# Optimization experiments

Measured on AMD Instinct MI355X. Metric: run time of the kernel, lower is better.

## Reference

```python
import jax, jax.numpy as jnp
import numpy as np

ALPHA = 0.25
GAMMA = 2.0


def calc_iou(a, b):
    # a: [A,4] anchors, b: [M,4] gt boxes -> IoU [A,M]
    area_b = (b[:, 2] - b[:, 0]) * (b[:, 3] - b[:, 1])
    iw = jnp.clip(jnp.minimum(a[:, None, 2], b[None, :, 2]) - jnp.maximum(a[:, None, 0], b[None, :, 0]), 0.0)
    ih = jnp.clip(jnp.minimum(a[:, None, 3], b[None, :, 3]) - jnp.maximum(a[:, None, 1], b[None, :, 1]), 0.0)
    inter = iw * ih
    area_a = (a[:, 2] - a[:, 0]) * (a[:, 3] - a[:, 1])
    ua = jnp.clip(area_a[:, None] + area_b[None, :] - inter, 1e-8)
    return inter / ua


def _per_image(classification, regression, annotation, anchor):
    valid = annotation[:, 4] != -1.0                      # padded GT mask
    has_valid = valid.any()
    cls = jnp.clip(classification, 1e-4, 1.0 - 1e-4)

    iou = calc_iou(anchor, annotation[:, :4])             # [A,M]
    iou = jnp.where(valid[None, :], iou, -1.0)            # mask padded GTs
    iou_max = iou.max(axis=1)
    iou_arg = iou.argmax(axis=1)
    assigned = annotation[iou_arg]                        # [A,5]

    pos = iou_max >= 0.5
    num_pos = pos.sum().astype(cls.dtype)

    K = classification.shape[1]
    t = jnp.full_like(classification, -1.0)
    t = jnp.where((iou_max < 0.4)[:, None], 0.0, t)
    onehot = jax.nn.one_hot(assigned[:, 4].astype(jnp.int32), K, dtype=cls.dtype)
    t = jnp.where(pos[:, None], onehot, t)

    alpha_factor = jnp.where(t == 1.0, ALPHA, 1.0 - ALPHA)
    focal_w = alpha_factor * jnp.where(t == 1.0, 1.0 - cls, cls) ** GAMMA
    bce = -(t * jnp.log(cls) + (1.0 - t) * jnp.log(1.0 - cls))
    cls_loss = jnp.where(t != -1.0, focal_w * bce, 0.0)
    cls_total = cls_loss.sum() / jnp.maximum(num_pos, 1.0)
    cls_total = jnp.where(has_valid, cls_total, 0.0)

    aw = anchor[:, 2] - anchor[:, 0]
    ah = anchor[:, 3] - anchor[:, 1]
    acx = anchor[:, 0] + 0.5 * aw
    acy = anchor[:, 1] + 0.5 * ah
    gw_raw = assigned[:, 2] - assigned[:, 0]
    gh_raw = assigned[:, 3] - assigned[:, 1]
    gcx = assigned[:, 0] + 0.5 * gw_raw                   # ctr uses unclamped w/h (as in torch)
    gcy = assigned[:, 1] + 0.5 * gh_raw
    gw = jnp.maximum(gw_raw, 1.0)
    gh = jnp.maximum(gh_raw, 1.0)
    tdx = (gcx - acx) / aw
    tdy = (gcy - acy) / ah
    tdw = jnp.log(gw / aw)
    tdh = jnp.log(gh / ah)
    norm = jnp.array([0.1, 0.1, 0.2, 0.2], dtype=cls.dtype)
    treg = jnp.stack([tdx, tdy, tdw, tdh], axis=1) / norm  # [A,4]

    diff = jnp.abs(treg - regression)
    sl1 = jnp.where(diff <= 1.0 / 9.0, 0.5 * 9.0 * diff ** 2, diff - 0.5 / 9.0)
    reg_sum = (sl1 * pos[:, None].astype(cls.dtype)).sum()
    reg_total = jnp.where(num_pos > 0.0, reg_sum / jnp.maximum(num_pos * 4.0, 1.0), 0.0)
    return cls_total, reg_total


def setup_inputs() -> dict:
    key = jax.random.key(0)
    k1, k2, k3, k4, k5, k6, k7 = jax.random.split(key, 7)
    B, A, K, M = 8, 120000, 80, 32
    classifications = jax.random.uniform(k1, (B, A, K), dtype=jnp.float32, minval=0.001, maxval=0.999)
    regressions = jax.random.normal(k2, (B, A, 4), dtype=jnp.float32)
    # anchors: valid x1y1x2y2 boxes in an ~800px image
    a_xy = jax.random.uniform(k3, (A, 2), dtype=jnp.float32, minval=0.0, maxval=600.0)
    a_wh = jax.random.uniform(k4, (A, 2), dtype=jnp.float32, minval=16.0, maxval=256.0)
    anchors = jnp.concatenate([a_xy, a_xy + a_wh], axis=1)[None]  # [1,A,4]
    # annotations: all valid GT boxes with class labels in [0,K)
    g_xy = jax.random.uniform(k5, (B, M, 2), dtype=jnp.float32, minval=0.0, maxval=500.0)
    g_wh = jax.random.uniform(k6, (B, M, 2), dtype=jnp.float32, minval=10.0, maxval=220.0)
    labels = jax.random.randint(k7, (B, M, 1), 0, K).astype(jnp.float32)
    annotations = jnp.concatenate([g_xy, g_xy + g_wh, labels], axis=2)  # [B,M,5]
    return {"classifications": classifications, "regressions": regressions,
            "anchors": anchors, "annotations": annotations}


def reference(classifications, regressions, anchors, annotations):
    anchor = anchors[0]
    cls_l, reg_l = jax.vmap(_per_image, in_axes=(0, 0, 0, None))(
        classifications, regressions, annotations, anchor)
    return cls_l.mean(keepdims=True), reg_l.mean(keepdims=True)
```

## Files before the change

### kernel.cpp

```cpp
#include <hip/hip_runtime.h>


__global__ __launch_bounds__(256) void stageA_kernel(
    const float* __restrict__ anchors,
    const float* __restrict__ regressions,
    const float* __restrict__ annotations,
    int* __restrict__ meta,
    float* __restrict__ reg_sum,
    unsigned int* __restrict__ npos,
    int A, int M)
{
    const int b = blockIdx.y;
    const int a = blockIdx.x * blockDim.x + threadIdx.x;

    __shared__ float ann[512];
    const int nl = M * 5;
    for (int i = threadIdx.x; i < nl; i += blockDim.x)
        ann[i] = annotations[b * nl + i];
    __syncthreads();

    float regl = 0.0f;
    float posf = 0.0f;

    if (a < A) {
        const float4 ab = *reinterpret_cast<const float4*>(anchors + (size_t)a * 4);
        const float aw = ab.z - ab.x, ah = ab.w - ab.y;
        const float areaA = aw * ah;

        float best = -3.0e38f;
        int arg = 0;
        for (int m = 0; m < M; ++m) {
            const float bx1 = ann[m * 5 + 0], by1 = ann[m * 5 + 1];
            const float bx2 = ann[m * 5 + 2], by2 = ann[m * 5 + 3];
            const float lb  = ann[m * 5 + 4];
            float iw = fmaxf(fminf(ab.z, bx2) - fmaxf(ab.x, bx1), 0.0f);
            float ih = fmaxf(fminf(ab.w, by2) - fmaxf(ab.y, by1), 0.0f);
            float inter = iw * ih;
            float ua = fmaxf(areaA + (bx2 - bx1) * (by2 - by1) - inter, 1e-8f);
            float iou = inter / ua;
            iou = (lb != -1.0f) ? iou : -1.0f;
            if (iou > best) { best = iou; arg = m; }
        }

        int mv;
        if (best >= 0.5f) {
            mv = (int)ann[arg * 5 + 4];
            posf = 1.0f;
            const float4 rg = *reinterpret_cast<const float4*>(
                regressions + ((size_t)b * A + a) * 4);
            const float gx1 = ann[arg * 5 + 0], gy1 = ann[arg * 5 + 1];
            const float gx2 = ann[arg * 5 + 2], gy2 = ann[arg * 5 + 3];
            const float acx = ab.x + 0.5f * aw, acy = ab.y + 0.5f * ah;
            const float gwr = gx2 - gx1, ghr = gy2 - gy1;
            const float gcx = gx1 + 0.5f * gwr, gcy = gy1 + 0.5f * ghr;
            const float gw = fmaxf(gwr, 1.0f), gh = fmaxf(ghr, 1.0f);
            const float t0 = ((gcx - acx) / aw) / 0.1f;
            const float t1 = ((gcy - acy) / ah) / 0.1f;
            const float t2 = logf(gw / aw) / 0.2f;
            const float t3 = logf(gh / ah) / 0.2f;
            const float d0 = fabsf(t0 - rg.x), d1 = fabsf(t1 - rg.y);
            const float d2 = fabsf(t2 - rg.z), d3 = fabsf(t3 - rg.w);
            const float th = 1.0f / 9.0f, c = 0.5f / 9.0f;
            regl  = (d0 <= th) ? 4.5f * d0 * d0 : d0 - c;
            regl += (d1 <= th) ? 4.5f * d1 * d1 : d1 - c;
            regl += (d2 <= th) ? 4.5f * d2 * d2 : d2 - c;
            regl += (d3 <= th) ? 4.5f * d3 * d3 : d3 - c;
        } else if (best < 0.4f) {
            mv = -1;
        } else {
            mv = -2;
        }
        meta[(size_t)b * A + a] = mv;
    }

    #pragma unroll
    for (int off = 32; off > 0; off >>= 1) {
        regl += __shfl_down(regl, off, 64);
        posf += __shfl_down(posf, off, 64);
    }
    __shared__ float wred[8];
    const int wave = threadIdx.x >> 6;
    const int lane = threadIdx.x & 63;
    if (lane == 0) { wred[wave] = regl; wred[4 + wave] = posf; }
    __syncthreads();
    if (threadIdx.x == 0) {
        const float r = wred[0] + wred[1] + wred[2] + wred[3];
        const float p = wred[4] + wred[5] + wred[6] + wred[7];
        if (r != 0.0f) atomicAdd(&reg_sum[b], r);
        if (p != 0.0f) atomicAdd(&npos[b], (unsigned int)p);
    }
}

template <int KV>
__global__ __launch_bounds__(256) void stageB_kernel(
    const float* __restrict__ cls,
    const int* __restrict__ meta,
    float* __restrict__ cls_sum,
    int A)
{
    const int b = blockIdx.y;
    const size_t nvec = (size_t)A * KV;
    const float4* __restrict__ base =
        reinterpret_cast<const float4*>(cls + (size_t)b * A * (KV * 4));
    const int* __restrict__ mbase = meta + (size_t)b * A;

    float acc = 0.0f;
    const unsigned int stride = gridDim.x * blockDim.x;
    for (size_t v = (size_t)blockIdx.x * blockDim.x + threadIdx.x; v < nvec; v += stride) {
        const float4 c4 = base[v];
        const unsigned int vu = (unsigned int)v;
        const int a = (int)(vu / KV);
        const int kbase = (int)(vu % KV) * 4;
        const int mv = mbase[a];
        if (mv != -2) {
            const float cv[4] = {c4.x, c4.y, c4.z, c4.w};
            #pragma unroll
            for (int j = 0; j < 4; ++j) {
                const float cc = fminf(fmaxf(cv[j], 1e-4f), 0.9999f);
                const bool t1 = (mv == kbase + j);
                const float x = t1 ? cc : (1.0f - cc);
                const float w = t1 ? 0.25f * (1.0f - cc) * (1.0f - cc)
                                   : 0.75f * cc * cc;
                acc += w * (-__logf(x));
            }
        }
    }

    #pragma unroll
    for (int off = 32; off > 0; off >>= 1)
        acc += __shfl_down(acc, off, 64);
    __shared__ float wred[4];
    const int wave = threadIdx.x >> 6;
    const int lane = threadIdx.x & 63;
    if (lane == 0) wred[wave] = acc;
    __syncthreads();
    if (threadIdx.x == 0)
        atomicAdd(&cls_sum[b], wred[0] + wred[1] + wred[2] + wred[3]);
}

__global__ __launch_bounds__(256) void stageB_generic(
    const float* __restrict__ cls, const int* __restrict__ meta,
    float* __restrict__ cls_sum, int A, int K)
{
    const int b = blockIdx.y;
    const int kv = K / 4;
    const size_t nvec = (size_t)A * kv;
    const float4* __restrict__ base =
        reinterpret_cast<const float4*>(cls + (size_t)b * A * K);
    const int* __restrict__ mbase = meta + (size_t)b * A;

    float acc = 0.0f;
    const unsigned int stride = gridDim.x * blockDim.x;
    for (size_t v = (size_t)blockIdx.x * blockDim.x + threadIdx.x; v < nvec; v += stride) {
        const float4 c4 = base[v];
        const int a = (int)(v / kv);
        const int kbase = (int)(v % kv) * 4;
        const int mv = mbase[a];
        if (mv != -2) {
            const float cv[4] = {c4.x, c4.y, c4.z, c4.w};
            #pragma unroll
            for (int j = 0; j < 4; ++j) {
                const float cc = fminf(fmaxf(cv[j], 1e-4f), 0.9999f);
                const bool t1 = (mv == kbase + j);
                const float x = t1 ? cc : (1.0f - cc);
                const float w = t1 ? 0.25f * (1.0f - cc) * (1.0f - cc)
                                   : 0.75f * cc * cc;
                acc += w * (-__logf(x));
            }
        }
    }

    #pragma unroll
    for (int off = 32; off > 0; off >>= 1)
        acc += __shfl_down(acc, off, 64);
    __shared__ float wred[4];
    const int wave = threadIdx.x >> 6;
    const int lane = threadIdx.x & 63;
    if (lane == 0) wred[wave] = acc;
    __syncthreads();
    if (threadIdx.x == 0)
        atomicAdd(&cls_sum[b], wred[0] + wred[1] + wred[2] + wred[3]);
}

__global__ void stageC_kernel(
    const float* __restrict__ annotations,
    const float* __restrict__ cls_sum,
    const float* __restrict__ reg_sum,
    const unsigned int* __restrict__ npos,
    float* __restrict__ out,
    int B, int M)
{
    if (threadIdx.x == 0 && blockIdx.x == 0) {
        float cm = 0.0f, rm = 0.0f;
        for (int b = 0; b < B; ++b) {
            bool hv = false;
            for (int m = 0; m < M; ++m)
                if (annotations[(b * M + m) * 5 + 4] != -1.0f) { hv = true; break; }
            const float np = (float)npos[b];
            float ct = cls_sum[b] / fmaxf(np, 1.0f);
            if (!hv) ct = 0.0f;
            const float rt = (np > 0.0f) ? reg_sum[b] / fmaxf(np * 4.0f, 1.0f) : 0.0f;
            cm += ct;
            rm += rt;
        }
        out[0] = cm / (float)B;
        out[1] = rm / (float)B;
    }
}

extern "C" void kernel_launch(void* const* d_in, const int* in_sizes, int n_in,
                              void* d_out, int out_size, void* d_ws, size_t ws_size,
                              hipStream_t stream) {
    const float* cls = (const float*)d_in[0];
    const float* reg = (const float*)d_in[1];
    const float* anc = (const float*)d_in[2];
    const float* ann = (const float*)d_in[3];

    const int A = in_sizes[2] / 4;
    const int B = in_sizes[1] / (A * 4);
    const int M = in_sizes[3] / (B * 5);
    const int K = in_sizes[0] / (B * A);

    float* out = (float*)d_out;
    float* cls_sum = (float*)d_ws;
    float* reg_sum = cls_sum + B;
    unsigned int* npos = (unsigned int*)(reg_sum + B);
    int* meta = (int*)((char*)d_ws + 256);

    hipMemsetAsync(d_ws, 0, 256, stream);

    dim3 ga((A + 255) / 256, B);
    stageA_kernel<<<ga, 256, 0, stream>>>(anc, reg, ann, meta, reg_sum, npos, A, M);

    dim3 gb(512, B);
    if (K == 80) {
        stageB_kernel<20><<<gb, 256, 0, stream>>>(cls, meta, cls_sum, A);
    } else {
        stageB_generic<<<gb, 256, 0, stream>>>(cls, meta, cls_sum, A, K);
    }

    stageC_kernel<<<1, 64, 0, stream>>>(ann, cls_sum, reg_sum, npos, out, B, M);
}
```

Baseline: 493.4 us.

## Fuse anchor matching and focal loss into one kernel with per-block partials

Merges the IoU/assignment stage and the classification-loss stage into a single kernel. Each block handles 256 anchors, keeps their assignment codes in shared memory, and then streams the matching classification rows. This drops the global meta array round trip, one kernel launch and the memset. Atomics are replaced by per-block partial sums that a parallel finalize kernel reduces. The cost is a grid sized by anchor chunks rather than a fixed 512 blocks, and each block's IoU loop serializes ahead of its streaming phase, which can reduce memory-level overlap.

```diff
diff --git a/kernel.cpp b/kernel.cpp
--- a/kernel.cpp
+++ b/kernel.cpp
@@ -1,27 +1,33 @@
 #include <hip/hip_runtime.h>
 
 
-__global__ __launch_bounds__(256) void stageA_kernel(
+#define CHUNK 256
+
+template <int KV>
+__global__ __launch_bounds__(256) void fused_kernel(
+    const float* __restrict__ cls,
+    const float* __restrict__ regr,
     const float* __restrict__ anchors,
-    const float* __restrict__ regressions,
-    const float* __restrict__ annotations,
-    int* __restrict__ meta,
-    float* __restrict__ reg_sum,
-    unsigned int* __restrict__ npos,
+    const float* __restrict__ ann_g,
+    float* __restrict__ pcls,
+    float* __restrict__ preg,
+    float* __restrict__ ppos,
     int A, int M)
 {
-    const int b = blockIdx.y;
-    const int a = blockIdx.x * blockDim.x + threadIdx.x;
+    const int b   = blockIdx.y;
+    const int blk = blockIdx.x;
+    const int a0  = blk * CHUNK;
+    const int tid = threadIdx.x;
 
     __shared__ float ann[512];
+    __shared__ int   smeta[CHUNK];
     const int nl = M * 5;
-    for (int i = threadIdx.x; i < nl; i += blockDim.x)
-        ann[i] = annotations[b * nl + i];
-    __syncthreads();
-
-    float regl = 0.0f;
-    float posf = 0.0f;
-
+    for (int i = tid; i < nl; i += 256) ann[i] = ann_g[b * nl + i];
+    __syncthreads();
+
+    float regl = 0.0f, posf = 0.0f;
+    int mv = -2;
+    const int a = a0 + tid;
     if (a < A) {
         const float4 ab = *reinterpret_cast<const float4*>(anchors + (size_t)a * 4);
         const float aw = ab.z - ab.x, ah = ab.w - ab.y;
@@ -42,12 +48,11 @@
             if (iou > best) { best = iou; arg = m; }
         }
 
-        int mv;
         if (best >= 0.5f) {
             mv = (int)ann[arg * 5 + 4];
             posf = 1.0f;
             const float4 rg = *reinterpret_cast<const float4*>(
-                regressions + ((size_t)b * A + a) * 4);
+                regr + ((size_t)b * A + a) * 4);
             const float gx1 = ann[arg * 5 + 0], gy1 = ann[arg * 5 + 1];
             const float gx2 = ann[arg * 5 + 2], gy2 = ann[arg * 5 + 3];
             const float acx = ab.x + 0.5f * aw, acy = ab.y + 0.5f * ah;
@@ -67,57 +72,28 @@
             regl += (d3 <= th) ? 4.5f * d3 * d3 : d3 - c;
         } else if (best < 0.4f) {
             mv = -1;
-        } else {
-            mv = -2;
-        }
-        meta[(size_t)b * A + a] = mv;
-    }
-
-    #pragma unroll
-    for (int off = 32; off > 0; off >>= 1) {
-        regl += __shfl_down(regl, off, 64);
-        posf += __shfl_down(posf, off, 64);
-    }
-    __shared__ float wred[8];
-    const int wave = threadIdx.x >> 6;
-    const int lane = threadIdx.x & 63;
-    if (lane == 0) { wred[wave] = regl; wred[4 + wave] = posf; }
-    __syncthreads();
-    if (threadIdx.x == 0) {
-        const float r = wred[0] + wred[1] + wred[2] + wred[3];
-        const float p = wred[4] + wred[5] + wred[6] + wred[7];
-        if (r != 0.0f) atomicAdd(&reg_sum[b], r);
-        if (p != 0.0f) atomicAdd(&npos[b], (unsigned int)p);
-    }
-}
-
-template <int KV>
-__global__ __launch_bounds__(256) void stageB_kernel(
-    const float* __restrict__ cls,
-    const int* __restrict__ meta,
-    float* __restrict__ cls_sum,
-    int A)
-{
-    const int b = blockIdx.y;
-    const size_t nvec = (size_t)A * KV;
+        }
+    }
+    smeta[tid] = mv;
+    __syncthreads();
+
+    const int span = min(CHUNK, A - a0);
+    const int nv = span * KV;
     const float4* __restrict__ base =
-        reinterpret_cast<const float4*>(cls + (size_t)b * A * (KV * 4));
-    const int* __restrict__ mbase = meta + (size_t)b * A;
+        reinterpret_cast<const float4*>(cls + ((size_t)b * A + a0) * (KV * 4));
 
     float acc = 0.0f;
-    const unsigned int stride = gridDim.x * blockDim.x;
-    for (size_t v = (size_t)blockIdx.x * blockDim.x + threadIdx.x; v < nvec; v += stride) {
-        const float4 c4 = base[v];
-        const unsigned int vu = (unsigned int)v;
-        const int a = (int)(vu / KV);
-        const int kbase = (int)(vu % KV) * 4;
-        const int mv = mbase[a];
-        if (mv != -2) {
+    for (int t = tid; t < nv; t += 256) {
+        const float4 c4 = base[t];
+        const int la    = t / KV;
+        const int kbase = (t % KV) * 4;
+        const int m2 = smeta[la];
+        if (m2 != -2) {
             const float cv[4] = {c4.x, c4.y, c4.z, c4.w};
             #pragma unroll
             for (int j = 0; j < 4; ++j) {
                 const float cc = fminf(fmaxf(cv[j], 1e-4f), 0.9999f);
-                const bool t1 = (mv == kbase + j);
+                const bool t1 = (m2 == kbase + j);
                 const float x = t1 ? cc : (1.0f - cc);
                 const float w = t1 ? 0.25f * (1.0f - cc) * (1.0f - cc)
                                    : 0.75f * cc * cc;
@@ -127,85 +103,162 @@
     }
 
     #pragma unroll
-    for (int off = 32; off > 0; off >>= 1)
-        acc += __shfl_down(acc, off, 64);
-    __shared__ float wred[4];
-    const int wave = threadIdx.x >> 6;
-    const int lane = threadIdx.x & 63;
-    if (lane == 0) wred[wave] = acc;
-    __syncthreads();
-    if (threadIdx.x == 0)
-        atomicAdd(&cls_sum[b], wred[0] + wred[1] + wred[2] + wred[3]);
-}
-
-__global__ __launch_bounds__(256) void stageB_generic(
-    const float* __restrict__ cls, const int* __restrict__ meta,
-    float* __restrict__ cls_sum, int A, int K)
+    for (int off = 32; off > 0; off >>= 1) {
+        acc  += __shfl_down(acc,  off, 64);
+        regl += __shfl_down(regl, off, 64);
+        posf += __shfl_down(posf, off, 64);
+    }
+    __shared__ float wred[12];
+    const int wave = tid >> 6, lane = tid & 63;
+    if (lane == 0) { wred[wave] = acc; wred[4 + wave] = regl; wred[8 + wave] = posf; }
+    __syncthreads();
+    if (tid == 0) {
+        const size_t o = (size_t)b * gridDim.x + blk;
+        pcls[o] = wred[0] + wred[1] + wred[2] + wred[3];
+        preg[o] = wred[4] + wred[5] + wred[6] + wred[7];
+        ppos[o] = wred[8] + wred[9] + wred[10] + wred[11];
+    }
+}
+
+__global__ __launch_bounds__(256) void fused_generic(
+    const float* __restrict__ cls, const float* __restrict__ regr,
+    const float* __restrict__ anchors, const float* __restrict__ ann_g,
+    float* __restrict__ pcls, float* __restrict__ preg, float* __restrict__ ppos,
+    int A, int M, int KV)
 {
-    const int b = blockIdx.y;
-    const int kv = K / 4;
-    const size_t nvec = (size_t)A * kv;
+    const int b   = blockIdx.y;
+    const int blk = blockIdx.x;
+    const int a0  = blk * CHUNK;
+    const int tid = threadIdx.x;
+
+    __shared__ float ann[512];
+    __shared__ int   smeta[CHUNK];
+    const int nl = M * 5;
+    for (int i = tid; i < nl; i += 256) ann[i] = ann_g[b * nl + i];
+    __syncthreads();
+
+    float regl = 0.0f, posf = 0.0f;
+    int mv = -2;
+    const int a = a0 + tid;
+    if (a < A) {
+        const float4 ab = *reinterpret_cast<const float4*>(anchors + (size_t)a * 4);
+        const float aw = ab.z - ab.x, ah = ab.w - ab.y;
+        const float areaA = aw * ah;
+        float best = -3.0e38f; int arg = 0;
+        for (int m = 0; m < M; ++m) {
+            const float bx1 = ann[m*5+0], by1 = ann[m*5+1];
+            const float bx2 = ann[m*5+2], by2 = ann[m*5+3];
+            const float lb  = ann[m*5+4];
+            float iw = fmaxf(fminf(ab.z, bx2) - fmaxf(ab.x, bx1), 0.0f);
+            float ih = fmaxf(fminf(ab.w, by2) - fmaxf(ab.y, by1), 0.0f);
+            float inter = iw * ih;
+            float ua = fmaxf(areaA + (bx2-bx1)*(by2-by1) - inter, 1e-8f);
+            float iou = inter / ua;
+            iou = (lb != -1.0f) ? iou : -1.0f;
+            if (iou > best) { best = iou; arg = m; }
+        }
+        if (best >= 0.5f) {
+            mv = (int)ann[arg*5+4]; posf = 1.0f;
+            const float4 rg = *reinterpret_cast<const float4*>(regr + ((size_t)b*A + a)*4);
+            const float gx1 = ann[arg*5+0], gy1 = ann[arg*5+1];
+            const float gx2 = ann[arg*5+2], gy2 = ann[arg*5+3];
+            const float acx = ab.x + 0.5f*aw, acy = ab.y + 0.5f*ah;
+            const float gwr = gx2-gx1, ghr = gy2-gy1;
+            const float gcx = gx1 + 0.5f*gwr, gcy = gy1 + 0.5f*ghr;
+            const float gw = fmaxf(gwr, 1.0f), gh = fmaxf(ghr, 1.0f);
+            const float t0 = ((gcx-acx)/aw)/0.1f, t1 = ((gcy-acy)/ah)/0.1f;
+            const float t2 = logf(gw/aw)/0.2f,    t3 = logf(gh/ah)/0.2f;
+            const float d0 = fabsf(t0-rg.x), d1 = fabsf(t1-rg.y);
+            const float d2 = fabsf(t2-rg.z), d3 = fabsf(t3-rg.w);
+            const float th = 1.0f/9.0f, c = 0.5f/9.0f;
+            regl  = (d0<=th)?4.5f*d0*d0:d0-c;  regl += (d1<=th)?4.5f*d1*d1:d1-c;
+            regl += (d2<=th)?4.5f*d2*d2:d2-c;  regl += (d3<=th)?4.5f*d3*d3:d3-c;
+        } else if (best < 0.4f) { mv = -1; }
+    }
+    smeta[tid] = mv;
+    __syncthreads();
+
+    const int span = min(CHUNK, A - a0);
+    const int nv = span * KV;
     const float4* __restrict__ base =
-        reinterpret_cast<const float4*>(cls + (size_t)b * A * K);
-    const int* __restrict__ mbase = meta + (size_t)b * A;
-
+        reinterpret_cast<const float4*>(cls + ((size_t)b*A + a0) * (KV*4));
     float acc = 0.0f;
-    const unsigned int stride = gridDim.x * blockDim.x;
-    for (size_t v = (size_t)blockIdx.x * blockDim.x + threadIdx.x; v < nvec; v += stride) {
-        const float4 c4 = base[v];
-        const int a = (int)(v / kv);
-        const int kbase = (int)(v % kv) * 4;
-        const int mv = mbase[a];
-        if (mv != -2) {
+    for (int t = tid; t < nv; t += 256) {
+        const float4 c4 = base[t];
+        const int la = t / KV, kbase = (t % KV) * 4;
+        const int m2 = smeta[la];
+        if (m2 != -2) {
             const float cv[4] = {c4.x, c4.y, c4.z, c4.w};
             #pragma unroll
             for (int j = 0; j < 4; ++j) {
                 const float cc = fminf(fmaxf(cv[j], 1e-4f), 0.9999f);
-                const bool t1 = (mv == kbase + j);
+                const bool t1 = (m2 == kbase + j);
                 const float x = t1 ? cc : (1.0f - cc);
-                const float w = t1 ? 0.25f * (1.0f - cc) * (1.0f - cc)
-                                   : 0.75f * cc * cc;
+                const float w = t1 ? 0.25f*(1.0f-cc)*(1.0f-cc) : 0.75f*cc*cc;
                 acc += w * (-__logf(x));
             }
         }
     }
 
     #pragma unroll
-    for (int off = 32; off > 0; off >>= 1)
-        acc += __shfl_down(acc, off, 64);
-    __shared__ float wred[4];
-    const int wave = threadIdx.x >> 6;
-    const int lane = threadIdx.x & 63;
-    if (lane == 0) wred[wave] = acc;
-    __syncthreads();
-    if (threadIdx.x == 0)
-        atomicAdd(&cls_sum[b], wred[0] + wred[1] + wred[2] + wred[3]);
-}
-
-__global__ void stageC_kernel(
-    const float* __restrict__ annotations,
-    const float* __restrict__ cls_sum,
-    const float* __restrict__ reg_sum,
-    const unsigned int* __restrict__ npos,
+    for (int off = 32; off > 0; off >>= 1) {
+        acc  += __shfl_down(acc,  off, 64);
+        regl += __shfl_down(regl, off, 64);
+        posf += __shfl_down(posf, off, 64);
+    }
+    __shared__ float wred[12];
+    const int wave = tid >> 6, lane = tid & 63;
+    if (lane == 0) { wred[wave] = acc; wred[4+wave] = regl; wred[8+wave] = posf; }
+    __syncthreads();
+    if (tid == 0) {
+        const size_t o = (size_t)b * gridDim.x + blk;
+        pcls[o] = wred[0]+wred[1]+wred[2]+wred[3];
+        preg[o] = wred[4]+wred[5]+wred[6]+wred[7];
+        ppos[o] = wred[8]+wred[9]+wred[10]+wred[11];
+    }
+}
+
+__global__ __launch_bounds__(256) void finalize_kernel(
+    const float* __restrict__ ann_g,
+    const float* __restrict__ pcls,
+    const float* __restrict__ preg,
+    const float* __restrict__ ppos,
     float* __restrict__ out,
-    int B, int M)
+    int B, int M, int nblk)
 {
-    if (threadIdx.x == 0 && blockIdx.x == 0) {
-        float cm = 0.0f, rm = 0.0f;
-        for (int b = 0; b < B; ++b) {
+    const int tid = threadIdx.x;
+    __shared__ float red[12];
+    float cm = 0.0f, rm = 0.0f;
+
+    for (int b = 0; b < B; ++b) {
+        float c = 0.0f, r = 0.0f, p = 0.0f;
+        for (int i = tid; i < nblk; i += 256) {
+            const size_t o = (size_t)b * nblk + i;
+            c += pcls[o]; r += preg[o]; p += ppos[o];
+        }
+        #pragma unroll
+        for (int off = 32; off > 0; off >>= 1) {
+            c += __shfl_down(c, off, 64);
+            r += __shfl_down(r, off, 64);
+            p += __shfl_down(p, off, 64);
+        }
+        const int wave = tid >> 6, lane = tid & 63;
+        if (lane == 0) { red[wave] = c; red[4+wave] = r; red[8+wave] = p; }
+        __syncthreads();
+        if (tid == 0) {
+            const float cs = red[0]+red[1]+red[2]+red[3];
+            const float rs = red[4]+red[5]+red[6]+red[7];
+            const float ps = red[8]+red[9]+red[10]+red[11];
             bool hv = false;
             for (int m = 0; m < M; ++m)
-                if (annotations[(b * M + m) * 5 + 4] != -1.0f) { hv = true; break; }
-            const float np = (float)npos[b];
-            float ct = cls_sum[b] / fmaxf(np, 1.0f);
-            if (!hv) ct = 0.0f;
-            const float rt = (np > 0.0f) ? reg_sum[b] / fmaxf(np * 4.0f, 1.0f) : 0.0f;
-            cm += ct;
-            rm += rt;
-        }
-        out[0] = cm / (float)B;
-        out[1] = rm / (float)B;
-    }
+                if (ann_g[((size_t)b * M + m) * 5 + 4] != -1.0f) { hv = true; break; }
+            const float ct = hv ? cs / fmaxf(ps, 1.0f) : 0.0f;
+            const float rt = (ps > 0.0f) ? rs / fmaxf(ps * 4.0f, 1.0f) : 0.0f;
+            cm += ct; rm += rt;
+        }
+        __syncthreads();
+    }
+    if (tid == 0) { out[0] = cm / (float)B; out[1] = rm / (float)B; }
 }
 
 extern "C" void kernel_launch(void* const* d_in, const int* in_sizes, int n_in,
@@ -220,24 +273,20 @@
     const int B = in_sizes[1] / (A * 4);
     const int M = in_sizes[3] / (B * 5);
     const int K = in_sizes[0] / (B * A);
+    const int nblk = (A + CHUNK - 1) / CHUNK;
 
     float* out = (float*)d_out;
-    float* cls_sum = (float*)d_ws;
-    float* reg_sum = cls_sum + B;
-    unsigned int* npos = (unsigned int*)(reg_sum + B);
-    int* meta = (int*)((char*)d_ws + 256);
-
-    hipMemsetAsync(d_ws, 0, 256, stream);
-
-    dim3 ga((A + 255) / 256, B);
-    stageA_kernel<<<ga, 256, 0, stream>>>(anc, reg, ann, meta, reg_sum, npos, A, M);
-
-    dim3 gb(512, B);
+    float* pcls = (float*)d_ws;
+    float* preg = pcls + (size_t)B * nblk;
+    float* ppos = preg + (size_t)B * nblk;
+
+    dim3 grid(nblk, B);
     if (K == 80) {
-        stageB_kernel<20><<<gb, 256, 0, stream>>>(cls, meta, cls_sum, A);
+        fused_kernel<20><<<grid, 256, 0, stream>>>(cls, reg, anc, ann,
+                                                   pcls, preg, ppos, A, M);
     } else {
-        stageB_generic<<<gb, 256, 0, stream>>>(cls, meta, cls_sum, A, K);
-    }
-
-    stageC_kernel<<<1, 64, 0, stream>>>(ann, cls_sum, reg_sum, npos, out, B, M);
-}
+        fused_generic<<<grid, 256, 0, stream>>>(cls, reg, anc, ann,
+                                                pcls, preg, ppos, A, M, K / 4);
+    }
+    finalize_kernel<<<1, 256, 0, stream>>>(ann, pcls, preg, ppos, out, B, M, nblk);
+}
```

Result: faster. 434.3 us (-12.0%).
